# Kernel optimization log

Measured on AMD Instinct MI355X. Metric: run time of the kernel, lower is better.

Reference implementation:

```python
import jax, jax.numpy as jnp
import numpy as np

N = 50000
E = 1600000
SI, SO, VI, VO, H, SVOD = 128, 128, 16, 16, 16, 3
EPS = 1e-8


def _safe_norm(x, axis, keepdims=False):
    return jnp.sqrt(jnp.sum(x * x, axis=axis, keepdims=keepdims) + EPS)


def setup_inputs() -> dict:
    key = jax.random.key(0)
    ks = jax.random.split(key, 13)

    def lin(k, fan_in, shape):
        b = 1.0 / np.sqrt(fan_in)
        return jax.random.uniform(k, shape, jnp.float32, -b, b)

    merged_dim = H + SI + 3 * SVOD  # 153
    return {
        "s": jax.random.normal(ks[0], (N, SI), jnp.float32),
        "v": jax.random.normal(ks[1], (N, VI, 3), jnp.float32),
        "frames": jax.random.normal(ks[2], (E, 3, 3), jnp.float32),
        "W_vd": lin(ks[3], VI, (VI, H)),            # vector_down (no bias)
        "W_vdf": lin(ks[4], VI, (VI, SVOD)),        # vector_down_frames (no bias)
        "W_so": lin(ks[5], merged_dim, (merged_dim, SO)),  # scalar_out
        "b_so": lin(ks[6], merged_dim, (SO,)),
        "W_vu": lin(ks[7], H, (H, VO)),             # vector_up (no bias)
        "W_vosf": lin(ks[8], SO, (SO, 3 * SVOD)),   # vector_out_scale_frames
        "b_vosf": lin(ks[9], SO, (3 * SVOD,)),
        "W_vuf": lin(ks[10], SVOD, (SVOD, VO)),     # vector_up_frames (no bias)
        "edge_index": jax.random.randint(ks[11], (2, E), 0, N, jnp.int32),
        "node_inputs": 1,
    }


def reference(s, v, frames, W_vd, W_vdf, W_so, b_so, W_vu, W_vosf, b_vosf, W_vuf, edge_index, node_inputs):
    # node_inputs is assumed truthy (node-wise GCP): gather by source node, scatter-mean back.
    row = edge_index[0]
    deg = jax.ops.segment_sum(jnp.ones((E,), s.dtype), row, num_segments=N)
    inv_deg = 1.0 / jnp.maximum(deg, 1.0)

    v_pre = jnp.swapaxes(v, -1, -2)                 # [N, 3, VI]
    vh = v_pre @ W_vd                                # [N, 3, H]
    vnorm = _safe_norm(vh, axis=-2)                  # [N, H]
    vdf = v_pre @ W_vdf                              # [N, 3, SVOD]

    # scalarize: project gathered source-node vectors onto per-edge frames, scatter-mean
    local = jnp.einsum('eij,ejc->eic', frames, vdf[row])       # [E, 3, SVOD]
    local9 = jnp.swapaxes(local, -1, -2).reshape(E, 3 * SVOD)  # [E, 9]
    sh = jax.ops.segment_sum(local9, row, num_segments=N) * inv_deg[:, None]  # [N, 9]

    merged = jnp.concatenate([s, vnorm, sh], axis=-1)          # [N, SI+H+9]
    scalar_rep = merged @ W_so + b_so                           # [N, SO]

    # vector path with frame gate
    vr = jnp.swapaxes(vh @ W_vu, -1, -2)                        # [N, VO, 3]
    gate = jax.nn.sigmoid(scalar_rep) @ W_vosf + b_vosf         # [N, 9]
    # vectorize: expand gate scalars back into vectors via frames, scatter-mean
    g = gate[row].reshape(E, 3, 3)
    gv_e = jnp.einsum('eji,ejk->eik', g, frames)                # [E, 3, 3]
    gv = jax.ops.segment_sum(gv_e, row, num_segments=N) * inv_deg[:, None, None]  # [N, 3, 3]
    gvr = jnp.swapaxes(jnp.swapaxes(gv, -1, -2) @ W_vuf, -1, -2)  # [N, VO, 3]
    vr = vr * jax.nn.sigmoid(_safe_norm(gvr, axis=-1, keepdims=True))

    return jax.nn.relu(scalar_rep), vr
```

## Files before the change

kernel.cpp:

```cpp
#include <hip/hip_runtime.h>

#define N_NODES 50000
#define N_EDGES 1600000
#define NPB     16
#define NCHAIN  16
#define MSTR    164
#define EPSV    1e-8f

typedef float f32x4 __attribute__((ext_vector_type(4)));
typedef short s16x8 __attribute__((ext_vector_type(8)));

struct f4u { float a, b, c, d; };

__device__ __forceinline__ float sigmoidf_(float x) { return 1.0f / (1.0f + __expf(-x)); }
__device__ __forceinline__ short f2bf(float x) {
    unsigned u = __float_as_uint(x);
    unsigned r = (u + 0x7FFFu + ((u >> 16) & 1u)) >> 16;
    return (short)r;
}
__device__ __forceinline__ float bf2f(short h) {
    return __uint_as_float(((unsigned)(unsigned short)h) << 16);
}

__global__ __launch_bounds__(256) void prep_w_kernel(
    const float* __restrict__ W_so, short* __restrict__ Whi, short* __restrict__ Wlo) {
    int i = blockIdx.x * 256 + threadIdx.x;
    if (i >= 160 * 128) return;
    int k = i >> 7;
    float w = (k < 153) ? W_so[i] : 0.0f;
    short hh = f2bf(w);
    Whi[i] = hh;
    Wlo[i] = f2bf(w - bf2f(hh));
}

__global__ __launch_bounds__(256) void bucket_kernel(
    const int* __restrict__ row,
    int* __restrict__ head,
    int* __restrict__ nxt) {
    int e = blockIdx.x * 256 + threadIdx.x;
    if (e >= N_EDGES) return;
    int r = row[e];
    int prev = atomicExch(&head[r * NCHAIN + (e & (NCHAIN - 1))], e);
    nxt[e] = prev;
}

__global__ __launch_bounds__(256) void node_kernel(
    const float* __restrict__ s,
    const float* __restrict__ v,
    const float* __restrict__ frames,
    const float* __restrict__ W_vd,
    const float* __restrict__ W_vdf,
    const short* __restrict__ Whi,
    const short* __restrict__ Wlo,
    const float* __restrict__ b_so,
    const float* __restrict__ W_vu,
    const float* __restrict__ W_vosf,
    const float* __restrict__ b_vosf,
    const float* __restrict__ W_vuf,
    const int* __restrict__ head,
    const int* __restrict__ nxt,
    float* __restrict__ out0,
    float* __restrict__ out1)
{
    __shared__ __align__(16) float poolL[NPB][MSTR];
    __shared__ float vL[NPB][48];
    __shared__ float vhL[NPB][3][16];
    __shared__ float FbarL[NPB][9];
    __shared__ float vdfL[NPB][9];
    __shared__ float gateL[NPB][12];

    float (*sigL)[128] = (float (*)[128])&poolL[0][0];

    const int t = threadIdx.x;
    const int base = blockIdx.x * NPB;
    const int nn = t >> 4, h = t & 15;
    const int n = base + nn;

    int e = head[(size_t)n * NCHAIN + h];

#pragma unroll
    for (int r = 0; r < 3; r++) vL[nn][h * 3 + r] = v[(size_t)n * 48 + h * 3 + r];
#pragma unroll
    for (int r = 0; r < 8; r++) poolL[nn][h * 8 + r] = s[(size_t)n * 128 + h * 8 + r];

    {
        float fs[10];
#pragma unroll
        for (int k = 0; k < 10; k++) fs[k] = 0.f;
        while (e >= 0) {
            int en = nxt[e];
            const float* f = frames + (size_t)e * 9;
            const f4u* fp = (const f4u*)f;
            f4u x = fp[0];
            f4u y = fp[1];
            float z8 = f[8];
            fs[0] += x.a; fs[1] += x.b; fs[2] += x.c; fs[3] += x.d;
            fs[4] += y.a; fs[5] += y.b; fs[6] += y.c; fs[7] += y.d;
            fs[8] += z8;
            fs[9] += 1.0f;
            e = en;
        }
#pragma unroll
        for (int m = 1; m < 16; m <<= 1) {
#pragma unroll
            for (int k = 0; k < 10; k++) fs[k] += __shfl_xor(fs[k], m);
        }
        if (h < 9) {
            float inv = 1.0f / fmaxf(fs[9], 1.0f);
            FbarL[nn][h] = fs[h] * inv;
        }
    }
    __syncthreads();

    {
        float vh0 = 0.f, vh1 = 0.f, vh2 = 0.f;
#pragma unroll
        for (int i = 0; i < 16; i++) {
            float w = W_vd[i * 16 + h];
            vh0 += vL[nn][i * 3 + 0] * w;
            vh1 += vL[nn][i * 3 + 1] * w;
            vh2 += vL[nn][i * 3 + 2] * w;
        }
        vhL[nn][0][h] = vh0; vhL[nn][1][h] = vh1; vhL[nn][2][h] = vh2;
        poolL[nn][128 + h] = sqrtf(vh0 * vh0 + vh1 * vh1 + vh2 * vh2 + EPSV);
        if (h < 3) {
            int cc = h;
#pragma unroll
            for (int j = 0; j < 3; j++) {
                float a = 0.f;
#pragma unroll
                for (int i = 0; i < 16; i++) a += vL[nn][i * 3 + j] * W_vdf[i * 3 + cc];
                vdfL[nn][j * 3 + cc] = a;
            }
        }
    }
    __syncthreads();

    {
        if (h < 9) {
            int c = h / 3, i = h % 3;
            float a = 0.f;
#pragma unroll
            for (int j = 0; j < 3; j++) a += FbarL[nn][i * 3 + j] * vdfL[nn][j * 3 + c];
            poolL[nn][144 + h] = a;
        } else {
            poolL[nn][144 + h] = 0.0f;
        }
        if (h < 4) poolL[nn][160 + h] = 0.0f;
    }
    __syncthreads();

    {
        const int w = t >> 6;
        const int lane = t & 63;
        const int quad = lane >> 4;
        const int col = lane & 15;
        f32x4 acc[2];
        acc[0] = (f32x4){0.f, 0.f, 0.f, 0.f};
        acc[1] = (f32x4){0.f, 0.f, 0.f, 0.f};
#pragma unroll
        for (int kk = 0; kk < 5; kk++) {
            const int krow = kk * 32 + quad * 8;
            const float* ap = &poolL[col][krow];
            float4 a0v = *(const float4*)ap;
            float4 a1v = *(const float4*)(ap + 4);
            float av[8] = {a0v.x, a0v.y, a0v.z, a0v.w, a1v.x, a1v.y, a1v.z, a1v.w};
            s16x8 ahi, alo;
#pragma unroll
            for (int j = 0; j < 8; j++) {
                short hh = f2bf(av[j]);
                ahi[j] = hh;
                alo[j] = f2bf(av[j] - bf2f(hh));
            }
#pragma unroll
            for (int t0 = 0; t0 < 2; t0++) {
                int o = w * 32 + t0 * 16 + col;
                s16x8 bhi, blo;
#pragma unroll
                for (int j = 0; j < 8; j++) {
                    bhi[j] = Whi[(krow + j) * 128 + o];
                    blo[j] = Wlo[(krow + j) * 128 + o];
                }
                acc[t0] = __builtin_amdgcn_mfma_f32_16x16x32_bf16(ahi, bhi, acc[t0], 0, 0, 0);
                acc[t0] = __builtin_amdgcn_mfma_f32_16x16x32_bf16(ahi, blo, acc[t0], 0, 0, 0);
                acc[t0] = __builtin_amdgcn_mfma_f32_16x16x32_bf16(alo, bhi, acc[t0], 0, 0, 0);
            }
        }
        __syncthreads();
#pragma unroll
        for (int t0 = 0; t0 < 2; t0++) {
            int o = w * 32 + t0 * 16 + col;
            float bso = b_so[o];
#pragma unroll
            for (int r = 0; r < 4; r++) {
                int nl = quad * 4 + r;
                float val = acc[t0][r] + bso;
                out0[(size_t)(base + nl) * 128 + o] = fmaxf(val, 0.0f);
                sigL[nl][o] = sigmoidf_(val);
            }
        }
    }
    __syncthreads();

    {
        const float* sp = &sigL[nn][h * 8];
        float4 s0 = *(const float4*)sp;
        float4 s1 = *(const float4*)(sp + 4);
        float sv[8] = {s0.x, s0.y, s0.z, s0.w, s1.x, s1.y, s1.z, s1.w};
        float p[9];
#pragma unroll
        for (int k = 0; k < 9; k++) p[k] = 0.f;
#pragma unroll
        for (int i = 0; i < 8; i++) {
            int o = h * 8 + i;
#pragma unroll
            for (int k = 0; k < 9; k++) p[k] += sv[i] * W_vosf[o * 9 + k];
        }
#pragma unroll
        for (int m = 1; m < 16; m <<= 1) {
#pragma unroll
            for (int k = 0; k < 9; k++) p[k] += __shfl_xor(p[k], m);
        }
        if (h < 9) gateL[nn][h] = p[h] + b_vosf[h];
    }
    __syncthreads();

    {
        int o = h;
        float gv[9];
#pragma unroll
        for (int i = 0; i < 3; i++)
#pragma unroll
            for (int kk = 0; kk < 3; kk++) {
                float a = 0.f;
#pragma unroll
                for (int j = 0; j < 3; j++) a += gateL[nn][j * 3 + i] * FbarL[nn][j * 3 + kk];
                gv[i * 3 + kk] = a;
            }
        float gvr[3];
#pragma unroll
        for (int kk = 0; kk < 3; kk++) {
            float a = 0.f;
#pragma unroll
            for (int i = 0; i < 3; i++) a += gv[i * 3 + kk] * W_vuf[i * 16 + o];
            gvr[kk] = a;
        }
        float gn2 = sqrtf(gvr[0] * gvr[0] + gvr[1] * gvr[1] + gvr[2] * gvr[2] + EPSV);
        float sg = sigmoidf_(gn2);
#pragma unroll
        for (int c = 0; c < 3; c++) {
            float a = 0.f;
#pragma unroll
            for (int h2 = 0; h2 < 16; h2++) a += vhL[nn][c][h2] * W_vu[h2 * 16 + o];
            out1[(size_t)n * 48 + o * 3 + c] = a * sg;
        }
    }
}

extern "C" void kernel_launch(void* const* d_in, const int* in_sizes, int n_in,
                              void* d_out, int out_size, void* d_ws, size_t ws_size,
                              hipStream_t stream) {
    const float* s      = (const float*)d_in[0];
    const float* v      = (const float*)d_in[1];
    const float* frames = (const float*)d_in[2];
    const float* W_vd   = (const float*)d_in[3];
    const float* W_vdf  = (const float*)d_in[4];
    const float* W_so   = (const float*)d_in[5];
    const float* b_so   = (const float*)d_in[6];
    const float* W_vu   = (const float*)d_in[7];
    const float* W_vosf = (const float*)d_in[8];
    const float* b_vosf = (const float*)d_in[9];
    const float* W_vuf  = (const float*)d_in[10];
    const int* edge_index = (const int*)d_in[11];

    const size_t head_b = (size_t)N_NODES * NCHAIN * sizeof(int);
    const size_t next_b = (size_t)N_EDGES * sizeof(int);
    int*   head = (int*)d_ws;
    int*   nxt  = (int*)((char*)d_ws + head_b);
    short* Whi  = (short*)((char*)d_ws + head_b + next_b);
    short* Wlo  = Whi + 160 * 128;
    float* out0 = (float*)d_out;
    float* out1 = out0 + (size_t)N_NODES * 128;

    hipMemsetAsync(head, 0xFF, head_b, stream);
    prep_w_kernel<<<(160 * 128 + 255) / 256, 256, 0, stream>>>(W_so, Whi, Wlo);
    bucket_kernel<<<(N_EDGES + 255) / 256, 256, 0, stream>>>(edge_index, head, nxt);
    node_kernel<<<N_NODES / NPB, 256, 0, stream>>>(
        s, v, frames, W_vd, W_vdf, Whi, Wlo, b_so, W_vu, W_vosf, b_vosf, W_vuf,
        head, nxt, out0, out1);
}
```

Before: 290.4 us.

## Pre-split activations to bf16 in LDS and transpose weights for vector loads

Activations are now split into bf16 hi/lo parts once, when they are written to shared memory, instead of being re-split inside the MFMA loop. W_so is stored transposed as [o][k] so each B fragment becomes a single 16-byte vector load rather than eight strided short loads. The head memset is folded into the weight-prep kernel, and launch bounds ask for 8 blocks per CU. In exchange, the sigmoid buffer aliasing the new short LDS array needs the array to stay large enough, and the per-node setup does more conversion work.

```diff
diff --git a/kernel.cpp b/kernel.cpp
--- a/kernel.cpp
+++ b/kernel.cpp
@@ -4,7 +4,7 @@
 #define N_EDGES 1600000
 #define NPB     16
 #define NCHAIN  16
-#define MSTR    164
+#define KSTR    168
 #define EPSV    1e-8f
 
 typedef float f32x4 __attribute__((ext_vector_type(4)));
@@ -22,15 +22,18 @@
     return __uint_as_float(((unsigned)(unsigned short)h) << 16);
 }
 
-__global__ __launch_bounds__(256) void prep_w_kernel(
-    const float* __restrict__ W_so, short* __restrict__ Whi, short* __restrict__ Wlo) {
+__global__ __launch_bounds__(256) void init_kernel(
+    const float* __restrict__ W_so, short* __restrict__ WThi, short* __restrict__ WTlo,
+    int* __restrict__ head) {
     int i = blockIdx.x * 256 + threadIdx.x;
-    if (i >= 160 * 128) return;
-    int k = i >> 7;
-    float w = (k < 153) ? W_so[i] : 0.0f;
-    short hh = f2bf(w);
-    Whi[i] = hh;
-    Wlo[i] = f2bf(w - bf2f(hh));
+    if (i < 128 * 160) {
+        int o = i / 160, k = i - o * 160;
+        float w = (k < 153) ? W_so[k * 128 + o] : 0.0f;
+        short hh = f2bf(w);
+        WThi[i] = hh;
+        WTlo[i] = f2bf(w - bf2f(hh));
+    }
+    if (i < N_NODES * NCHAIN) head[i] = -1;
 }
 
 __global__ __launch_bounds__(256) void bucket_kernel(
@@ -44,14 +47,14 @@
     nxt[e] = prev;
 }
 
-__global__ __launch_bounds__(256) void node_kernel(
+__global__ __launch_bounds__(256, 8) void node_kernel(
     const float* __restrict__ s,
     const float* __restrict__ v,
     const float* __restrict__ frames,
     const float* __restrict__ W_vd,
     const float* __restrict__ W_vdf,
-    const short* __restrict__ Whi,
-    const short* __restrict__ Wlo,
+    const short* __restrict__ WThi,
+    const short* __restrict__ WTlo,
     const float* __restrict__ b_so,
     const float* __restrict__ W_vu,
     const float* __restrict__ W_vosf,
@@ -62,14 +65,14 @@
     float* __restrict__ out0,
     float* __restrict__ out1)
 {
-    __shared__ __align__(16) float poolL[NPB][MSTR];
+    __shared__ __align__(16) short AL[2][NPB][KSTR];
     __shared__ float vL[NPB][48];
     __shared__ float vhL[NPB][3][16];
     __shared__ float FbarL[NPB][9];
     __shared__ float vdfL[NPB][9];
     __shared__ float gateL[NPB][12];
 
-    float (*sigL)[128] = (float (*)[128])&poolL[0][0];
+    float (*sigL)[128] = (float (*)[128])&AL[0][0][0];
 
     const int t = threadIdx.x;
     const int base = blockIdx.x * NPB;
@@ -80,8 +83,20 @@
 
 #pragma unroll
     for (int r = 0; r < 3; r++) vL[nn][h * 3 + r] = v[(size_t)n * 48 + h * 3 + r];
-#pragma unroll
-    for (int r = 0; r < 8; r++) poolL[nn][h * 8 + r] = s[(size_t)n * 128 + h * 8 + r];
+    {
+        const float4* sp4 = (const float4*)(s + (size_t)n * 128 + h * 8);
+        float4 s0 = sp4[0], s1 = sp4[1];
+        float sv[8] = {s0.x, s0.y, s0.z, s0.w, s1.x, s1.y, s1.z, s1.w};
+        s16x8 shi, slo;
+#pragma unroll
+        for (int j = 0; j < 8; j++) {
+            short hh = f2bf(sv[j]);
+            shi[j] = hh;
+            slo[j] = f2bf(sv[j] - bf2f(hh));
+        }
+        *(s16x8*)&AL[0][nn][h * 8] = shi;
+        *(s16x8*)&AL[1][nn][h * 8] = slo;
+    }
 
     {
         float fs[10];
@@ -122,7 +137,10 @@
             vh2 += vL[nn][i * 3 + 2] * w;
         }
         vhL[nn][0][h] = vh0; vhL[nn][1][h] = vh1; vhL[nn][2][h] = vh2;
-        poolL[nn][128 + h] = sqrtf(vh0 * vh0 + vh1 * vh1 + vh2 * vh2 + EPSV);
+        float vn = sqrtf(vh0 * vh0 + vh1 * vh1 + vh2 * vh2 + EPSV);
+        short hh = f2bf(vn);
+        AL[0][nn][128 + h] = hh;
+        AL[1][nn][128 + h] = f2bf(vn - bf2f(hh));
         if (h < 3) {
             int cc = h;
 #pragma unroll
@@ -142,11 +160,13 @@
             float a = 0.f;
 #pragma unroll
             for (int j = 0; j < 3; j++) a += FbarL[nn][i * 3 + j] * vdfL[nn][j * 3 + c];
-            poolL[nn][144 + h] = a;
+            short hh = f2bf(a);
+            AL[0][nn][144 + h] = hh;
+            AL[1][nn][144 + h] = f2bf(a - bf2f(hh));
         } else {
-            poolL[nn][144 + h] = 0.0f;
-        }
-        if (h < 4) poolL[nn][160 + h] = 0.0f;
+            AL[0][nn][144 + h] = 0;
+            AL[1][nn][144 + h] = 0;
+        }
     }
     __syncthreads();
 
@@ -155,48 +175,37 @@
         const int lane = t & 63;
         const int quad = lane >> 4;
         const int col = lane & 15;
-        f32x4 acc[2];
-        acc[0] = (f32x4){0.f, 0.f, 0.f, 0.f};
-        acc[1] = (f32x4){0.f, 0.f, 0.f, 0.f};
+        const int o0 = w * 32 + col, o1 = o0 + 16;
+        f32x4 acc0 = (f32x4){0.f, 0.f, 0.f, 0.f};
+        f32x4 acc1 = (f32x4){0.f, 0.f, 0.f, 0.f};
 #pragma unroll
         for (int kk = 0; kk < 5; kk++) {
             const int krow = kk * 32 + quad * 8;
-            const float* ap = &poolL[col][krow];
-            float4 a0v = *(const float4*)ap;
-            float4 a1v = *(const float4*)(ap + 4);
-            float av[8] = {a0v.x, a0v.y, a0v.z, a0v.w, a1v.x, a1v.y, a1v.z, a1v.w};
-            s16x8 ahi, alo;
-#pragma unroll
-            for (int j = 0; j < 8; j++) {
-                short hh = f2bf(av[j]);
-                ahi[j] = hh;
-                alo[j] = f2bf(av[j] - bf2f(hh));
-            }
-#pragma unroll
-            for (int t0 = 0; t0 < 2; t0++) {
-                int o = w * 32 + t0 * 16 + col;
-                s16x8 bhi, blo;
-#pragma unroll
-                for (int j = 0; j < 8; j++) {
-                    bhi[j] = Whi[(krow + j) * 128 + o];
-                    blo[j] = Wlo[(krow + j) * 128 + o];
-                }
-                acc[t0] = __builtin_amdgcn_mfma_f32_16x16x32_bf16(ahi, bhi, acc[t0], 0, 0, 0);
-                acc[t0] = __builtin_amdgcn_mfma_f32_16x16x32_bf16(ahi, blo, acc[t0], 0, 0, 0);
-                acc[t0] = __builtin_amdgcn_mfma_f32_16x16x32_bf16(alo, bhi, acc[t0], 0, 0, 0);
-            }
+            s16x8 ahi = *(const s16x8*)&AL[0][col][krow];
+            s16x8 alo = *(const s16x8*)&AL[1][col][krow];
+            s16x8 b0h = *(const s16x8*)&WThi[o0 * 160 + krow];
+            s16x8 b0l = *(const s16x8*)&WTlo[o0 * 160 + krow];
+            s16x8 b1h = *(const s16x8*)&WThi[o1 * 160 + krow];
+            s16x8 b1l = *(const s16x8*)&WTlo[o1 * 160 + krow];
+            acc0 = __builtin_amdgcn_mfma_f32_16x16x32_bf16(ahi, b0h, acc0, 0, 0, 0);
+            acc0 = __builtin_amdgcn_mfma_f32_16x16x32_bf16(ahi, b0l, acc0, 0, 0, 0);
+            acc0 = __builtin_amdgcn_mfma_f32_16x16x32_bf16(alo, b0h, acc0, 0, 0, 0);
+            acc1 = __builtin_amdgcn_mfma_f32_16x16x32_bf16(ahi, b1h, acc1, 0, 0, 0);
+            acc1 = __builtin_amdgcn_mfma_f32_16x16x32_bf16(ahi, b1l, acc1, 0, 0, 0);
+            acc1 = __builtin_amdgcn_mfma_f32_16x16x32_bf16(alo, b1h, acc1, 0, 0, 0);
         }
         __syncthreads();
-#pragma unroll
-        for (int t0 = 0; t0 < 2; t0++) {
-            int o = w * 32 + t0 * 16 + col;
-            float bso = b_so[o];
+        {
+            float b0 = b_so[o0], b1 = b_so[o1];
 #pragma unroll
             for (int r = 0; r < 4; r++) {
                 int nl = quad * 4 + r;
-                float val = acc[t0][r] + bso;
-                out0[(size_t)(base + nl) * 128 + o] = fmaxf(val, 0.0f);
-                sigL[nl][o] = sigmoidf_(val);
+                float v0 = acc0[r] + b0;
+                float v1 = acc1[r] + b1;
+                out0[(size_t)(base + nl) * 128 + o0] = fmaxf(v0, 0.0f);
+                out0[(size_t)(base + nl) * 128 + o1] = fmaxf(v1, 0.0f);
+                sigL[nl][o0] = sigmoidf_(v0);
+                sigL[nl][o1] = sigmoidf_(v1);
             }
         }
     }
@@ -277,15 +286,14 @@
     const size_t next_b = (size_t)N_EDGES * sizeof(int);
     int*   head = (int*)d_ws;
     int*   nxt  = (int*)((char*)d_ws + head_b);
-    short* Whi  = (short*)((char*)d_ws + head_b + next_b);
-    short* Wlo  = Whi + 160 * 128;
+    short* WThi = (short*)((char*)d_ws + head_b + next_b);
+    short* WTlo = WThi + 128 * 160;
     float* out0 = (float*)d_out;
     float* out1 = out0 + (size_t)N_NODES * 128;
 
-    hipMemsetAsync(head, 0xFF, head_b, stream);
-    prep_w_kernel<<<(160 * 128 + 255) / 256, 256, 0, stream>>>(W_so, Whi, Wlo);
+    init_kernel<<<(N_NODES * NCHAIN + 255) / 256, 256, 0, stream>>>(W_so, WThi, WTlo, head);
     bucket_kernel<<<(N_EDGES + 255) / 256, 256, 0, stream>>>(edge_index, head, nxt);
     node_kernel<<<N_NODES / NPB, 256, 0, stream>>>(
-        s, v, frames, W_vd, W_vdf, Whi, Wlo, b_so, W_vu, W_vosf, b_vosf, W_vuf,
+        s, v, frames, W_vd, W_vdf, WThi, WTlo, b_so, W_vu, W_vosf, b_vosf, W_vuf,
         head, nxt, out0, out1);
 }
```

Measured after the change: 294.5 us. No clear change (+1.4%).
